# Kernel tuning notes

Measured on AMD Instinct MI355X. Metric: run time of the kernel, lower is better.

The kernel has to match this reference:

```python
import jax, jax.numpy as jnp
import numpy as np

NEG_INF = -1e9


def setup_inputs() -> dict:
    key = jax.random.key(0)
    ks = jax.random.split(key, 6)
    B, S, E, D = 32, 2048, 1024, 1024
    dec_hidden = jax.random.normal(ks[0], (B, D), dtype=jnp.float32)
    enc_outputs = jax.random.normal(ks[1], (B, S, E), dtype=jnp.float32)
    mask = jax.random.randint(ks[2], (B, S), 0, 2, dtype=jnp.int32)
    # scale weights ~ Glorot-ish so tanh isn't saturated
    W_enc = jax.random.normal(ks[3], (D, E), dtype=jnp.float32) / np.sqrt(E)
    W_dec = jax.random.normal(ks[4], (D, D), dtype=jnp.float32) / np.sqrt(D)
    v = jax.random.normal(ks[5], (D,), dtype=jnp.float32) / np.sqrt(D)
    return {"dec_hidden": dec_hidden, "enc_outputs": enc_outputs, "mask": mask,
            "W_enc": W_enc, "W_dec": W_dec, "v": v}


def reference(dec_hidden, enc_outputs, mask, W_enc, W_dec, v):
    # dh: [B, D]  (torch Linear: x @ W.T)
    dh = dec_hidden @ W_dec.T
    # eh: [B, S, D]
    eh = jnp.einsum('bse,de->bsd', enc_outputs, W_enc)
    # additive energy + projection by v -> scores [B, S]
    energy = jnp.tanh(dh[:, None, :] + eh)
    scores = jnp.einsum('bsd,d->bs', energy, v)
    scores = jnp.where(mask == 0, NEG_INF, scores)
    weights = jax.nn.softmax(scores, axis=1)          # [B, S]
    context = jnp.einsum('bs,bse->be', weights, enc_outputs)  # [B, E]
    return context, weights
```

## Files before the change

kernel.cpp:

```cpp
#include <hip/hip_runtime.h>
#include <stdint.h>

typedef float f32x4 __attribute__((ext_vector_type(4)));
typedef float f32x16 __attribute__((ext_vector_type(16)));
typedef short bf16x8 __attribute__((ext_vector_type(8)));
typedef unsigned short ushort8 __attribute__((ext_vector_type(8)));

__device__ __forceinline__ unsigned short f2bf(float x) {
  union { float f; uint32_t u; } c; c.f = x;
  return (unsigned short)((c.u + 0x8000u) >> 16);
}
__device__ __forceinline__ float bf2f(unsigned short u) {
  union { uint32_t u; float f; } c; c.u = ((uint32_t)u) << 16;
  return c.f;
}

__global__ void prep_w4_k(const float* __restrict__ W, unsigned short* __restrict__ Wt) {
  int t = blockIdx.x * 256 + threadIdx.x;
  int d  = t >> 7;
  int c0 = (t & 127) << 3;
  const float* src = W + ((size_t)d << 10) + c0;
  f32x4 f0 = *(const f32x4*)src;
  f32x4 f1 = *(const f32x4*)(src + 4);
  ushort8 u;
  u[0]=f2bf(f0[0]); u[1]=f2bf(f0[1]); u[2]=f2bf(f0[2]); u[3]=f2bf(f0[3]);
  u[4]=f2bf(f1[0]); u[5]=f2bf(f1[1]); u[6]=f2bf(f1[2]); u[7]=f2bf(f1[3]);
  int nt = d >> 7, r = d & 127;
  int kt = c0 >> 5;
  int q  = ((c0 & 31) >> 3) ^ ((r >> 1) & 3);
  Wt += (((size_t)(nt * 32 + kt)) << 12) + r * 32 + q * 8;
  *(ushort8*)Wt = u;
}

__global__ void prep_dh_k(const float* __restrict__ dec, const float* __restrict__ Wd,
                          float* __restrict__ dh) {
  __shared__ float sdec[1024];
  int b = blockIdx.x >> 2;
  for (int i = threadIdx.x; i < 1024; i += 256) sdec[i] = dec[(b << 10) + i];
  __syncthreads();
  int d = ((blockIdx.x & 3) << 8) + threadIdx.x;
  const float* wr = Wd + ((size_t)d << 10);
  float a = 0.f;
  for (int k = 0; k < 1024; k += 4) {
    f32x4 wv = *(const f32x4*)(wr + k);
    f32x4 xv = *(const f32x4*)(&sdec[k]);
    a += wv[0]*xv[0] + wv[1]*xv[1] + wv[2]*xv[2] + wv[3]*xv[3];
  }
  dh[(b << 10) + d] = a;
}

__global__ void compact_k(const int* __restrict__ mask, int* __restrict__ rows,
                          int* __restrict__ cnt, float* __restrict__ wout) {
  int b = blockIdx.x, tid = threadIdx.x;
  int lane = tid & 63, wv = tid >> 6;
  int mloc[8]; int c = 0;
  #pragma unroll
  for (int ii = 0; ii < 8; ++ii) {
    int s = tid * 8 + ii;
    int m = mask[(b << 11) + s];
    mloc[ii] = m; c += m;
    wout[(b << 11) + s] = 0.f;
  }
  int inc = c;
  #pragma unroll
  for (int off = 1; off < 64; off <<= 1) {
    int nn = __shfl_up(inc, off);
    if (lane >= off) inc += nn;
  }
  __shared__ int wsum[4];
  if (lane == 63) wsum[wv] = inc;
  __syncthreads();
  int base = 0;
  for (int w = 0; w < wv; ++w) base += wsum[w];
  int idx = base + inc - c;
  #pragma unroll
  for (int ii = 0; ii < 8; ++ii) {
    if (mloc[ii]) { rows[(b << 11) + idx] = tid * 8 + ii; ++idx; }
  }
  if (tid == 0) cnt[b] = wsum[0] + wsum[1] + wsum[2] + wsum[3];
}

__global__ void pack4_k(const float* __restrict__ enc, const int* __restrict__ rows,
                        const int* __restrict__ cnt, unsigned short* __restrict__ encP) {
  int b = blockIdx.x >> 4, mt = blockIdx.x & 15;
  int n = cnt[b];
  if (mt * 128 >= n) return;
  __shared__ int sr[128];
  if (threadIdx.x < 128) {
    int i = mt * 128 + threadIdx.x; if (i >= n) i = n - 1;
    sr[threadIdx.x] = rows[(b << 11) + i];
  }
  __syncthreads();
  unsigned short* dst = encP + (((size_t)(b * 16 + mt)) << 17);
  for (int it = 0; it < 64; ++it) {
    int idx = it * 256 + threadIdx.x;
    int r   = idx >> 7;
    int c0  = (idx & 127) << 3;
    const float* src = enc + (((size_t)(b << 11) + sr[r]) << 10) + c0;
    f32x4 f0 = *(const f32x4*)src;
    f32x4 f1 = *(const f32x4*)(src + 4);
    ushort8 u;
    u[0]=f2bf(f0[0]); u[1]=f2bf(f0[1]); u[2]=f2bf(f0[2]); u[3]=f2bf(f0[3]);
    u[4]=f2bf(f1[0]); u[5]=f2bf(f1[1]); u[6]=f2bf(f1[2]); u[7]=f2bf(f1[3]);
    int kt = c0 >> 5;
    int q  = ((c0 & 31) >> 3) ^ ((r >> 1) & 3);
    *(ushort8*)(dst + (kt << 12) + r * 32 + q * 8) = u;
  }
}

__global__ __launch_bounds__(256, 3) void score4_k(
    const unsigned short* __restrict__ encP, const unsigned short* __restrict__ Wt,
    const float* __restrict__ dh, const float* __restrict__ v,
    const int* __restrict__ cnt, float* __restrict__ pscores)
{
  int L  = (blockIdx.x & 7) * 512 + (blockIdx.x >> 3);
  int b  = L >> 7, mt = (L >> 3) & 15, nt = L & 7;
  int n  = cnt[b];
  if (mt * 128 >= n) return;

  __shared__ __align__(16) unsigned short AS[2][4096];
  __shared__ __align__(16) unsigned short BS[2][4096];
  __shared__ float sc[128][2];

  int tid  = threadIdx.x;
  int lane = tid & 63;
  int wv   = tid >> 6;
  int wm = wv >> 1, wn = wv & 1;
  int l31 = lane & 31, l5 = lane >> 5;

  const unsigned short* aT = encP + (((size_t)(b * 16 + mt)) << 17);
  const unsigned short* bT = Wt + (((size_t)nt) << 17);

  int offA[2][2], offB[2][2];
  #pragma unroll
  for (int mf = 0; mf < 2; ++mf) {
    int r = wm * 64 + mf * 32 + l31;
    #pragma unroll
    for (int ki = 0; ki < 2; ++ki)
      offA[mf][ki] = r * 32 + (((ki * 2 + l5) ^ ((r >> 1) & 3)) << 3);
  }
  #pragma unroll
  for (int nf = 0; nf < 2; ++nf) {
    int r = wn * 64 + nf * 32 + l31;
    #pragma unroll
    for (int ki = 0; ki < 2; ++ki)
      offB[nf][ki] = r * 32 + (((ki * 2 + l5) ^ ((r >> 1) & 3)) << 3);
  }

  f32x16 acc[2][2];
  #pragma unroll
  for (int i = 0; i < 2; ++i)
    #pragma unroll
    for (int j = 0; j < 2; ++j)
      #pragma unroll
      for (int e = 0; e < 16; ++e)
        acc[i][j][e] = 0.f;

  auto stage = [&](int slot, int kt) {
    #pragma unroll
    for (int j = 0; j < 2; ++j) {
      int chunk = wv * 2 + j;
      __builtin_amdgcn_global_load_lds(
        (const __attribute__((address_space(1))) void*)(const void*)(aT + ((size_t)kt << 12) + chunk * 512 + lane * 8),
        (__attribute__((address_space(3))) void*)(void*)(&AS[slot][chunk * 512]), 16, 0, 0);
      __builtin_amdgcn_global_load_lds(
        (const __attribute__((address_space(1))) void*)(const void*)(bT + ((size_t)kt << 12) + chunk * 512 + lane * 8),
        (__attribute__((address_space(3))) void*)(void*)(&BS[slot][chunk * 512]), 16, 0, 0);
    }
  };

  auto compute = [&](int slot) {
    bf16x8 af[2][2], bf[2][2];
    #pragma unroll
    for (int mf = 0; mf < 2; ++mf)
      #pragma unroll
      for (int ki = 0; ki < 2; ++ki)
        af[mf][ki] = *(const bf16x8*)&AS[slot][offA[mf][ki]];
    #pragma unroll
    for (int nf = 0; nf < 2; ++nf)
      #pragma unroll
      for (int ki = 0; ki < 2; ++ki)
        bf[nf][ki] = *(const bf16x8*)&BS[slot][offB[nf][ki]];
    #pragma unroll
    for (int ki = 0; ki < 2; ++ki)
      #pragma unroll
      for (int mf = 0; mf < 2; ++mf)
        #pragma unroll
        for (int nf = 0; nf < 2; ++nf)
          acc[mf][nf] = __builtin_amdgcn_mfma_f32_32x32x16_bf16(af[mf][ki], bf[nf][ki], acc[mf][nf], 0, 0, 0);
  };

  stage(0, 0);
  __syncthreads();
  int slot = 0;
  for (int kt = 0; kt < 31; ++kt) {
    stage(slot ^ 1, kt + 1);
    compute(slot);
    __syncthreads();
    slot ^= 1;
  }
  compute(slot);

  float vv[2], dd[2];
  #pragma unroll
  for (int nf = 0; nf < 2; ++nf) {
    int dcol = nt * 128 + wn * 64 + nf * 32 + l31;
    vv[nf] = v[dcol];
    dd[nf] = dh[(b << 10) + dcol];
  }
  #pragma unroll
  for (int mf = 0; mf < 2; ++mf) {
    #pragma unroll
    for (int reg = 0; reg < 16; ++reg) {
      float p = 0.f;
      #pragma unroll
      for (int nf = 0; nf < 2; ++nf) {
        float x = acc[mf][nf][reg] + dd[nf];
        float e = __expf(2.0f * x);
        float t = 1.0f - __fdividef(2.0f, e + 1.0f);
        p += vv[nf] * t;
      }
      p += __shfl_xor(p, 1); p += __shfl_xor(p, 2); p += __shfl_xor(p, 4);
      p += __shfl_xor(p, 8); p += __shfl_xor(p, 16);
      if (l31 == 0) {
        int row = wm * 64 + mf * 32 + (reg & 3) + 8 * (reg >> 2) + 4 * l5;
        sc[row][wn] = p;
      }
    }
  }
  __syncthreads();
  if (tid < 128) {
    int i = mt * 128 + tid;
    if (i < n)
      pscores[(((size_t)nt) << 16) + (b << 11) + i] = sc[tid][0] + sc[tid][1];
  }
}

__global__ void softmax4_k(const float* __restrict__ ps, const int* __restrict__ rows,
                           const int* __restrict__ cnt, float* __restrict__ wout,
                           float* __restrict__ wc) {
  int b = blockIdx.x;
  int tid = threadIdx.x;
  int n = cnt[b];
  float val[8];
  float m = -INFINITY;
  #pragma unroll
  for (int ii = 0; ii < 8; ++ii) {
    int i = tid + ii * 256;
    float s = -INFINITY;
    if (i < n) {
      s = 0.f;
      #pragma unroll
      for (int nt = 0; nt < 8; ++nt) s += ps[(((size_t)nt) << 16) + (b << 11) + i];
    }
    val[ii] = s;
    m = fmaxf(m, s);
  }
  #pragma unroll
  for (int off = 1; off < 64; off <<= 1) m = fmaxf(m, __shfl_xor(m, off));
  __shared__ float r1[4], r2[4];
  if ((tid & 63) == 0) r1[tid >> 6] = m;
  __syncthreads();
  m = fmaxf(fmaxf(r1[0], r1[1]), fmaxf(r1[2], r1[3]));
  float ssum = 0.f;
  #pragma unroll
  for (int ii = 0; ii < 8; ++ii) { val[ii] = __expf(val[ii] - m); ssum += val[ii]; }
  #pragma unroll
  for (int off = 1; off < 64; off <<= 1) ssum += __shfl_xor(ssum, off);
  if ((tid & 63) == 0) r2[tid >> 6] = ssum;
  __syncthreads();
  ssum = r2[0] + r2[1] + r2[2] + r2[3];
  float inv = 1.0f / ssum;
  #pragma unroll
  for (int ii = 0; ii < 8; ++ii) {
    int i = tid + ii * 256;
    if (i < n) {
      float w = val[ii] * inv;
      wc[(b << 11) + i] = w;
      wout[((size_t)b << 11) + rows[(b << 11) + i]] = w;
    }
  }
}

__global__ void ctx4_k(const unsigned short* __restrict__ encP, const float* __restrict__ wc,
                       const int* __restrict__ cnt, float* __restrict__ cp) {
  int b = blockIdx.x >> 4, mt = blockIdx.x & 15;
  int n = cnt[b];
  float* out = cp + (((size_t)(b * 16 + mt)) << 10);
  int tid = threadIdx.x;
  if (mt * 128 >= n) {
    #pragma unroll
    for (int j = 0; j < 4; ++j) out[tid * 4 + j] = 0.f;
    return;
  }
  __shared__ float sw[128];
  __shared__ float red[128][8];
  if (tid < 128) {
    int i = mt * 128 + tid;
    sw[tid] = (i < n) ? wc[(b << 11) + i] : 0.f;
  }
  __syncthreads();
  const unsigned short* tile = encP + (((size_t)(b * 16 + mt)) << 17);
  int cb8  = tid & 127;
  int half = tid >> 7;
  int kt = cb8 >> 2, q0 = cb8 & 3;
  float a[8];
  #pragma unroll
  for (int j = 0; j < 8; ++j) a[j] = 0.f;
  for (int rr = 0; rr < 64; ++rr) {
    int r = half * 64 + rr;
    float w = sw[r];
    ushort8 u = *(const ushort8*)(tile + (kt << 12) + r * 32 + ((q0 ^ ((r >> 1) & 3)) << 3));
    #pragma unroll
    for (int j = 0; j < 8; ++j) a[j] += w * bf2f(u[j]);
  }
  if (half == 1) {
    #pragma unroll
    for (int j = 0; j < 8; ++j) red[cb8][j] = a[j];
  }
  __syncthreads();
  if (half == 0) {
    #pragma unroll
    for (int j = 0; j < 8; ++j) out[cb8 * 8 + j] = a[j] + red[cb8][j];
  }
}

__global__ void ctx_red4_k(const float* __restrict__ cp, float* __restrict__ out) {
  int t = blockIdx.x * 256 + threadIdx.x;
  int b = t >> 10, e = t & 1023;
  float a = 0.f;
  #pragma unroll
  for (int mt = 0; mt < 16; ++mt) a += cp[(((size_t)(b * 16 + mt)) << 10) + e];
  out[t] = a;
}

extern "C" void kernel_launch(void* const* d_in, const int* in_sizes, int n_in,
                              void* d_out, int out_size, void* d_ws, size_t ws_size,
                              hipStream_t stream) {
  const float* dec  = (const float*)d_in[0];
  const float* enc  = (const float*)d_in[1];
  const int*   mask = (const int*)d_in[2];
  const float* Wenc = (const float*)d_in[3];
  const float* Wdec = (const float*)d_in[4];
  const float* v    = (const float*)d_in[5];
  float* out_ctx = (float*)d_out;
  float* out_w   = (float*)d_out + 32768;

  char* ws = (char*)d_ws;
  unsigned short* Wt = (unsigned short*)ws;
  float* dh    = (float*)(ws + (2u << 20));
  int*   rows  = (int*)(ws + (2u << 20) + (128u << 10));
  float* wc    = (float*)(ws + (2u << 20) + (384u << 10));
  int*   cnt   = (int*)(ws + (2u << 20) + (640u << 10));
  float* pscores = (float*)(ws + (3u << 20));
  float* cp      = (float*)(ws + (5u << 20));
  unsigned short* encP = (unsigned short*)(ws + (8ull << 20));

  hipLaunchKernelGGL(prep_w4_k,  dim3(512),  dim3(256), 0, stream, Wenc, Wt);
  hipLaunchKernelGGL(prep_dh_k,  dim3(128),  dim3(256), 0, stream, dec, Wdec, dh);
  hipLaunchKernelGGL(compact_k,  dim3(32),   dim3(256), 0, stream, mask, rows, cnt, out_w);
  hipLaunchKernelGGL(pack4_k,    dim3(512),  dim3(256), 0, stream, enc, rows, cnt, encP);
  hipLaunchKernelGGL(score4_k,   dim3(4096), dim3(256), 0, stream, encP, Wt, dh, v, cnt, pscores);
  hipLaunchKernelGGL(softmax4_k, dim3(32),   dim3(256), 0, stream, pscores, rows, cnt, out_w, wc);
  hipLaunchKernelGGL(ctx4_k,     dim3(512),  dim3(256), 0, stream, encP, wc, cnt, cp);
  hipLaunchKernelGGL(ctx_red4_k, dim3(128),  dim3(256), 0, stream, cp, out_ctx);
}
```

Measured before the change: 217.8 us.

## Widen score GEMM tile to 128x256 with triple-buffered LDS pipeline

```diff
diff --git a/kernel.cpp b/kernel.cpp
--- a/kernel.cpp
+++ b/kernel.cpp
@@ -15,7 +15,7 @@
   return c.f;
 }
 
-__global__ void prep_w4_k(const float* __restrict__ W, unsigned short* __restrict__ Wt) {
+__global__ void prep_w5_k(const float* __restrict__ W, unsigned short* __restrict__ Wt) {
   int t = blockIdx.x * 256 + threadIdx.x;
   int d  = t >> 7;
   int c0 = (t & 127) << 3;
@@ -25,11 +25,10 @@
   ushort8 u;
   u[0]=f2bf(f0[0]); u[1]=f2bf(f0[1]); u[2]=f2bf(f0[2]); u[3]=f2bf(f0[3]);
   u[4]=f2bf(f1[0]); u[5]=f2bf(f1[1]); u[6]=f2bf(f1[2]); u[7]=f2bf(f1[3]);
-  int nt = d >> 7, r = d & 127;
+  int ntp = d >> 8, rr = d & 255;
   int kt = c0 >> 5;
-  int q  = ((c0 & 31) >> 3) ^ ((r >> 1) & 3);
-  Wt += (((size_t)(nt * 32 + kt)) << 12) + r * 32 + q * 8;
-  *(ushort8*)Wt = u;
+  int q  = ((c0 & 31) >> 3) ^ ((rr >> 1) & 3);
+  *(ushort8*)(Wt + (((size_t)ntp) << 18) + kt * 8192 + rr * 32 + q * 8) = u;
 }
 
 __global__ void prep_dh_k(const float* __restrict__ dec, const float* __restrict__ Wd,
@@ -108,18 +107,22 @@
   }
 }
 
-__global__ __launch_bounds__(256, 3) void score4_k(
+#define GLOAD16(g, l) __builtin_amdgcn_global_load_lds( \
+    (const __attribute__((address_space(1))) void*)(const void*)(g), \
+    (__attribute__((address_space(3))) void*)(void*)(l), 16, 0, 0)
+
+__global__ __launch_bounds__(256) void score5_k(
     const unsigned short* __restrict__ encP, const unsigned short* __restrict__ Wt,
     const float* __restrict__ dh, const float* __restrict__ v,
     const int* __restrict__ cnt, float* __restrict__ pscores)
 {
-  int L  = (blockIdx.x & 7) * 512 + (blockIdx.x >> 3);
-  int b  = L >> 7, mt = (L >> 3) & 15, nt = L & 7;
+  int L  = (blockIdx.x & 7) * 256 + (blockIdx.x >> 3);
+  int b  = L >> 6, mt = (L >> 2) & 15, ntp = L & 3;
   int n  = cnt[b];
   if (mt * 128 >= n) return;
 
-  __shared__ __align__(16) unsigned short AS[2][4096];
-  __shared__ __align__(16) unsigned short BS[2][4096];
+  __shared__ __align__(16) unsigned short AS[3][4096];
+  __shared__ __align__(16) unsigned short BS[3][8192];
   __shared__ float sc[128][2];
 
   int tid  = threadIdx.x;
@@ -129,9 +132,9 @@
   int l31 = lane & 31, l5 = lane >> 5;
 
   const unsigned short* aT = encP + (((size_t)(b * 16 + mt)) << 17);
-  const unsigned short* bT = Wt + (((size_t)nt) << 17);
-
-  int offA[2][2], offB[2][2];
+  const unsigned short* bT = Wt + (((size_t)ntp) << 18);
+
+  int offA[2][2], offB[4][2];
   #pragma unroll
   for (int mf = 0; mf < 2; ++mf) {
     int r = wm * 64 + mf * 32 + l31;
@@ -140,18 +143,18 @@
       offA[mf][ki] = r * 32 + (((ki * 2 + l5) ^ ((r >> 1) & 3)) << 3);
   }
   #pragma unroll
-  for (int nf = 0; nf < 2; ++nf) {
-    int r = wn * 64 + nf * 32 + l31;
+  for (int nf = 0; nf < 4; ++nf) {
+    int r = wn * 128 + nf * 32 + l31;
     #pragma unroll
     for (int ki = 0; ki < 2; ++ki)
       offB[nf][ki] = r * 32 + (((ki * 2 + l5) ^ ((r >> 1) & 3)) << 3);
   }
 
-  f32x16 acc[2][2];
+  f32x16 acc[2][4];
   #pragma unroll
   for (int i = 0; i < 2; ++i)
     #pragma unroll
-    for (int j = 0; j < 2; ++j)
+    for (int j = 0; j < 4; ++j)
       #pragma unroll
       for (int e = 0; e < 16; ++e)
         acc[i][j][e] = 0.f;
@@ -160,24 +163,24 @@
     #pragma unroll
     for (int j = 0; j < 2; ++j) {
       int chunk = wv * 2 + j;
-      __builtin_amdgcn_global_load_lds(
-        (const __attribute__((address_space(1))) void*)(const void*)(aT + ((size_t)kt << 12) + chunk * 512 + lane * 8),
-        (__attribute__((address_space(3))) void*)(void*)(&AS[slot][chunk * 512]), 16, 0, 0);
-      __builtin_amdgcn_global_load_lds(
-        (const __attribute__((address_space(1))) void*)(const void*)(bT + ((size_t)kt << 12) + chunk * 512 + lane * 8),
-        (__attribute__((address_space(3))) void*)(void*)(&BS[slot][chunk * 512]), 16, 0, 0);
+      GLOAD16(aT + ((size_t)kt << 12) + chunk * 512 + lane * 8, &AS[slot][chunk * 512]);
+    }
+    #pragma unroll
+    for (int j = 0; j < 4; ++j) {
+      int chunk = wv * 4 + j;
+      GLOAD16(bT + ((size_t)kt << 13) + chunk * 512 + lane * 8, &BS[slot][chunk * 512]);
     }
   };
 
   auto compute = [&](int slot) {
-    bf16x8 af[2][2], bf[2][2];
+    bf16x8 af[2][2], bf[4][2];
     #pragma unroll
     for (int mf = 0; mf < 2; ++mf)
       #pragma unroll
       for (int ki = 0; ki < 2; ++ki)
         af[mf][ki] = *(const bf16x8*)&AS[slot][offA[mf][ki]];
     #pragma unroll
-    for (int nf = 0; nf < 2; ++nf)
+    for (int nf = 0; nf < 4; ++nf)
       #pragma unroll
       for (int ki = 0; ki < 2; ++ki)
         bf[nf][ki] = *(const bf16x8*)&BS[slot][offB[nf][ki]];
@@ -186,25 +189,38 @@
       #pragma unroll
       for (int mf = 0; mf < 2; ++mf)
         #pragma unroll
-        for (int nf = 0; nf < 2; ++nf)
+        for (int nf = 0; nf < 4; ++nf)
           acc[mf][nf] = __builtin_amdgcn_mfma_f32_32x32x16_bf16(af[mf][ki], bf[nf][ki], acc[mf][nf], 0, 0, 0);
   };
 
+#define K_STEP(SLOT, SSLOT, KTS, FENCE)                                   \
+  {                                                                       \
+    if ((KTS) >= 0) stage((SSLOT), (KTS));                                \
+    if constexpr ((FENCE) == 12) asm volatile("s_waitcnt vmcnt(12)" ::: "memory"); \
+    else if constexpr ((FENCE) == 6) asm volatile("s_waitcnt vmcnt(6)" ::: "memory"); \
+    else asm volatile("s_waitcnt vmcnt(0)" ::: "memory");                 \
+    __builtin_amdgcn_s_barrier();                                         \
+    __builtin_amdgcn_sched_barrier(0);                                    \
+    compute(SLOT);                                                        \
+    __builtin_amdgcn_s_barrier();                                         \
+  }
+
   stage(0, 0);
-  __syncthreads();
-  int slot = 0;
-  for (int kt = 0; kt < 31; ++kt) {
-    stage(slot ^ 1, kt + 1);
-    compute(slot);
-    __syncthreads();
-    slot ^= 1;
-  }
-  compute(slot);
-
-  float vv[2], dd[2];
-  #pragma unroll
-  for (int nf = 0; nf < 2; ++nf) {
-    int dcol = nt * 128 + wn * 64 + nf * 32 + l31;
+  stage(1, 1);
+  #pragma unroll 1
+  for (int t = 0; t < 30; t += 3) {
+    K_STEP(0, 2, t + 2, 12)
+    K_STEP(1, 0, t + 3, 12)
+    K_STEP(2, 1, t + 4, 12)
+  }
+  K_STEP(0, 0, -1, 6)
+  K_STEP(1, 0, -1, 0)
+#undef K_STEP
+
+  float vv[4], dd[4];
+  #pragma unroll
+  for (int nf = 0; nf < 4; ++nf) {
+    int dcol = ntp * 256 + wn * 128 + nf * 32 + l31;
     vv[nf] = v[dcol];
     dd[nf] = dh[(b << 10) + dcol];
   }
@@ -214,7 +230,7 @@
     for (int reg = 0; reg < 16; ++reg) {
       float p = 0.f;
       #pragma unroll
-      for (int nf = 0; nf < 2; ++nf) {
+      for (int nf = 0; nf < 4; ++nf) {
         float x = acc[mf][nf][reg] + dd[nf];
         float e = __expf(2.0f * x);
         float t = 1.0f - __fdividef(2.0f, e + 1.0f);
@@ -232,11 +248,11 @@
   if (tid < 128) {
     int i = mt * 128 + tid;
     if (i < n)
-      pscores[(((size_t)nt) << 16) + (b << 11) + i] = sc[tid][0] + sc[tid][1];
-  }
-}
-
-__global__ void softmax4_k(const float* __restrict__ ps, const int* __restrict__ rows,
+      pscores[(((size_t)ntp) << 16) + (b << 11) + i] = sc[tid][0] + sc[tid][1];
+  }
+}
+
+__global__ void softmax5_k(const float* __restrict__ ps, const int* __restrict__ rows,
                            const int* __restrict__ cnt, float* __restrict__ wout,
                            float* __restrict__ wc) {
   int b = blockIdx.x;
@@ -251,7 +267,7 @@
     if (i < n) {
       s = 0.f;
       #pragma unroll
-      for (int nt = 0; nt < 8; ++nt) s += ps[(((size_t)nt) << 16) + (b << 11) + i];
+      for (int nt = 0; nt < 4; ++nt) s += ps[(((size_t)nt) << 16) + (b << 11) + i];
     }
     val[ii] = s;
     m = fmaxf(m, s);
@@ -356,12 +372,12 @@
   float* cp      = (float*)(ws + (5u << 20));
   unsigned short* encP = (unsigned short*)(ws + (8ull << 20));
 
-  hipLaunchKernelGGL(prep_w4_k,  dim3(512),  dim3(256), 0, stream, Wenc, Wt);
+  hipLaunchKernelGGL(prep_w5_k,  dim3(512),  dim3(256), 0, stream, Wenc, Wt);
   hipLaunchKernelGGL(prep_dh_k,  dim3(128),  dim3(256), 0, stream, dec, Wdec, dh);
   hipLaunchKernelGGL(compact_k,  dim3(32),   dim3(256), 0, stream, mask, rows, cnt, out_w);
   hipLaunchKernelGGL(pack4_k,    dim3(512),  dim3(256), 0, stream, enc, rows, cnt, encP);
-  hipLaunchKernelGGL(score4_k,   dim3(4096), dim3(256), 0, stream, encP, Wt, dh, v, cnt, pscores);
-  hipLaunchKernelGGL(softmax4_k, dim3(32),   dim3(256), 0, stream, pscores, rows, cnt, out_w, wc);
+  hipLaunchKernelGGL(score5_k,   dim3(2048), dim3(256), 0, stream, encP, Wt, dh, v, cnt, pscores);
+  hipLaunchKernelGGL(softmax5_k, dim3(32),   dim3(256), 0, stream, pscores, rows, cnt, out_w, wc);
   hipLaunchKernelGGL(ctx4_k,     dim3(512),  dim3(256), 0, stream, encP, wc, cnt, cp);
   hipLaunchKernelGGL(ctx_red4_k, dim3(128),  dim3(256), 0, stream, cp, out_ctx);
 }
```

After: 280.6 us. 1.29x slower.
